# Kernel tuning notes

Measured on AMD Instinct MI355X. Metric: run time of the kernel, lower is better.

Reference implementation:

```python
import jax, jax.numpy as jnp
import numpy as np

EMB = 512
HEADS = 8


def setup_inputs() -> dict:
    key = jax.random.key(0)
    ks = jax.random.split(key, 9)
    b, t, k, h = 4, 2048, EMB, HEADS
    s = 1.0 / np.sqrt(k)
    x = jax.random.normal(ks[0], (b, t, k), dtype=jnp.float32)
    Wq = jax.random.normal(ks[1], (k, h * k), dtype=jnp.float32) * s
    bq = jnp.zeros((h * k,), dtype=jnp.float32)
    Wk = jax.random.normal(ks[2], (k, h * k), dtype=jnp.float32) * s
    bk = jnp.zeros((h * k,), dtype=jnp.float32)
    Wv = jax.random.normal(ks[3], (k, h * k), dtype=jnp.float32) * s
    bv = jnp.zeros((h * k,), dtype=jnp.float32)
    Wo = jax.random.normal(ks[4], (h * k, k), dtype=jnp.float32) * (1.0 / np.sqrt(h * k))
    bo = jnp.zeros((k,), dtype=jnp.float32)
    return {"x": x, "Wq": Wq, "bq": bq, "Wk": Wk, "bk": bk,
            "Wv": Wv, "bv": bv, "Wo": Wo, "bo": bo}


def reference(x, Wq, bq, Wk, bk, Wv, bv, Wo, bo):
    b, t, k = x.shape
    h = Wq.shape[1] // k
    scale = k ** (-0.25)  # applied to both q and k, matching /= k**(1/4)
    # projections: [b,t,k] -> [b,t,h,k] -> [b,h,t,k]
    q = (x @ Wq + bq).reshape(b, t, h, k).transpose(0, 2, 1, 3) * scale
    kk = (x @ Wk + bk).reshape(b, t, h, k).transpose(0, 2, 1, 3) * scale
    v = (x @ Wv + bv).reshape(b, t, h, k).transpose(0, 2, 1, 3)
    # attention scores [b,h,t,t]
    scores = jnp.einsum('bhqk,bhsk->bhqs', q, kk)
    w = jax.nn.softmax(scores, axis=-1)
    out = jnp.einsum('bhqs,bhsk->bhqk', w, v)  # [b,h,t,k]
    out = out.transpose(0, 2, 1, 3).reshape(b, t, h * k)
    return out @ Wo + bo
```

## Files before the change

kernel.cpp:

```cpp
#include <hip/hip_runtime.h>
#include <hip/hip_bf16.h>
#include <stdint.h>

typedef __hip_bfloat16 bf16;
typedef __bf16 bf16x8 __attribute__((ext_vector_type(8)));
typedef float floatx4 __attribute__((ext_vector_type(4)));

#define AS_LDS __attribute__((address_space(3)))
#define AS_GLB __attribute__((address_space(1)))

__device__ __forceinline__ void gload_lds16(const bf16* g, bf16* l) {
    __builtin_amdgcn_global_load_lds((const AS_GLB void*)g, (AS_LDS void*)l, 16, 0, 0);
}

__global__ void probe_dtype(const float* __restrict__ x, int* __restrict__ flag) {
    __shared__ int cnt;
    if (threadIdx.x == 0) cnt = 0;
    __syncthreads();
    int ok = 0;
    for (int i = threadIdx.x; i < 4096; i += 256) {
        float v = x[i];
        if (v == v && fabsf(v) < 1.0e3f) ok++;
    }
    atomicAdd(&cnt, ok);
    __syncthreads();
    if (threadIdx.x == 0) *flag = (cnt > 2048) ? 1 : 0;
}

__global__ __launch_bounds__(256) void convert_to_bf16(
    const void* __restrict__ in, bf16* __restrict__ out, long n,
    const int* __restrict__ flag)
{
    long i = ((long)blockIdx.x * 256 + threadIdx.x) * 8;
    if (i >= n) return;
    bf16 o[8];
    if (*flag) {
        const float* p = (const float*)in + i;
        float4 a = *(const float4*)p;
        float4 b = *(const float4*)(p + 4);
        o[0] = __float2bfloat16(a.x); o[1] = __float2bfloat16(a.y);
        o[2] = __float2bfloat16(a.z); o[3] = __float2bfloat16(a.w);
        o[4] = __float2bfloat16(b.x); o[5] = __float2bfloat16(b.y);
        o[6] = __float2bfloat16(b.z); o[7] = __float2bfloat16(b.w);
    } else {
        *(float4*)o = *(const float4*)((const bf16*)in + i);
    }
    *(float4*)&out[i] = *(float4*)o;
}

__global__ __launch_bounds__(256) void emit_out(
    const bf16* __restrict__ in, void* __restrict__ out, long n,
    const int* __restrict__ flag)
{
    long i = ((long)blockIdx.x * 256 + threadIdx.x) * 8;
    if (i >= n) return;
    bf16 v[8];
    *(float4*)v = *(const float4*)&in[i];
    if (*flag) {
        float* o = (float*)out + i;
        float4 a, b;
        a.x = __bfloat162float(v[0]); a.y = __bfloat162float(v[1]);
        a.z = __bfloat162float(v[2]); a.w = __bfloat162float(v[3]);
        b.x = __bfloat162float(v[4]); b.y = __bfloat162float(v[5]);
        b.z = __bfloat162float(v[6]); b.w = __bfloat162float(v[7]);
        *(float4*)o = a;
        *(float4*)(o + 4) = b;
    } else {
        *(float4*)((bf16*)out + i) = *(float4*)v;
    }
}

__global__ __launch_bounds__(256) void transpose_any(
    const void* __restrict__ inv, bf16* __restrict__ out,
    int ldin, int ldout, const int* __restrict__ flag)
{
    __shared__ bf16 tile[64][80];
    const int fp32 = *flag;
    const int c0 = blockIdx.x * 64;
    const int r0 = blockIdx.y * 64;
    const int tid = threadIdx.x;
#pragma unroll
    for (int it = 0; it < 2; ++it) {
        int ch = tid + it * 256;
        int r = ch >> 3, c = (ch & 7) * 8;
        long eidx = (long)(r0 + r) * ldin + (c0 + c);
        if (fp32) {
            const float* p = (const float*)inv + eidx;
            float4 a = *(const float4*)p;
            float4 b = *(const float4*)(p + 4);
            bf16 o[8];
            o[0] = __float2bfloat16(a.x); o[1] = __float2bfloat16(a.y);
            o[2] = __float2bfloat16(a.z); o[3] = __float2bfloat16(a.w);
            o[4] = __float2bfloat16(b.x); o[5] = __float2bfloat16(b.y);
            o[6] = __float2bfloat16(b.z); o[7] = __float2bfloat16(b.w);
            *(float4*)&tile[r][c] = *(float4*)o;
        } else {
            *(float4*)&tile[r][c] = *(const float4*)((const bf16*)inv + eidx);
        }
    }
    __syncthreads();
#pragma unroll
    for (int it = 0; it < 2; ++it) {
        int ch = tid + it * 256;
        int oc = ch >> 3, rb = (ch & 7) * 8;
        bf16 tmp[8];
#pragma unroll
        for (int i = 0; i < 8; ++i) tmp[i] = tile[rb + i][oc];
        *(float4*)&out[(long)(c0 + oc) * ldout + r0 + rb] = *(float4*)tmp;
    }
}

__global__ __launch_bounds__(256) void transpose_bf16(
    const bf16* __restrict__ in, bf16* __restrict__ out,
    int ldin, int ldout,
    int nz1, long in_z1, long out_z1, long in_z2, long out_z2)
{
    __shared__ bf16 tile[64][80];
    const int z = blockIdx.z;
    const int z1 = z % nz1, z2 = z / nz1;
    in  += (long)z1 * in_z1 + (long)z2 * in_z2;
    out += (long)z1 * out_z1 + (long)z2 * out_z2;
    const int c0 = blockIdx.x * 64;
    const int r0 = blockIdx.y * 64;
    const int tid = threadIdx.x;
#pragma unroll
    for (int it = 0; it < 2; ++it) {
        int ch = tid + it * 256;
        int r = ch >> 3, c = (ch & 7) * 8;
        *(float4*)&tile[r][c] = *(const float4*)&in[(long)(r0 + r) * ldin + c0 + c];
    }
    __syncthreads();
#pragma unroll
    for (int it = 0; it < 2; ++it) {
        int ch = tid + it * 256;
        int oc = ch >> 3, rb = (ch & 7) * 8;
        bf16 tmp[8];
#pragma unroll
        for (int i = 0; i < 8; ++i) tmp[i] = tile[rb + i][oc];
        *(float4*)&out[(long)(c0 + oc) * ldout + r0 + rb] = *(float4*)tmp;
    }
}

template <int MODE>
__global__ __launch_bounds__(512, 2) void gemm256(
    const bf16* __restrict__ A, const bf16* __restrict__ Bt,
    bf16* __restrict__ C, const bf16* __restrict__ bias,
    int lda, int ldb, int ldc,
    long az, long bz, long cz, int K, float scale, int qcols,
    bf16* __restrict__ Vt, int vcol0)
{
    __shared__ bf16 AsL[2][2][256 * 32];
    __shared__ bf16 BsL[2][2][256 * 32];

    const int tid  = threadIdx.x;
    const int lane = tid & 63;
    const int wave = tid >> 6;
    const int wr = wave >> 2;
    const int wc = wave & 3;
    const int lm = lane & 15;
    const int cl = lane >> 4;
    const long zz = blockIdx.z;
    A  += zz * az;
    Bt += zz * bz;
    C  += zz * cz;
    const int m0 = blockIdx.y * 256;
    const int n0 = blockIdx.x * 256;

    int offA[8], offB[4];
#pragma unroll
    for (int i = 0; i < 8; ++i) {
        int row = wr * 128 + i * 16 + lm;
        offA[i] = row * 32 + ((cl ^ ((row >> 1) & 3)) << 3);
    }
#pragma unroll
    for (int j = 0; j < 4; ++j) {
        int row = wc * 64 + j * 16 + lm;
        offB[j] = row * 32 + ((cl ^ ((row >> 1) & 3)) << 3);
    }

    const int sr = lane >> 2;
    const int sc = lane & 3;
    const int NT = K >> 6;

    floatx4 acc[8][4];
#pragma unroll
    for (int i = 0; i < 8; ++i)
#pragma unroll
        for (int j = 0; j < 4; ++j)
            acc[i][j] = (floatx4){0.f, 0.f, 0.f, 0.f};

    auto stageU = [&](int which, int t, int kh) {
        if (t >= NT) return;
        const bf16* G = which ? Bt : A;
        const int ldg  = which ? ldb : lda;
        const int g0   = which ? n0 : m0;
        bf16* lb = which ? &BsL[t & 1][kh][0] : &AsL[t & 1][kh][0];
        const int kcol = t * 64 + kh * 32;
#pragma unroll
        for (int ii = 0; ii < 2; ++ii) {
            int row = ii * 128 + wave * 16 + sr;
            int cg  = sc ^ ((row >> 1) & 3);
            gload_lds16(G + (long)(g0 + row) * ldg + kcol + cg * 8,
                        lb + row * 32 + sc * 8);
        }
    };

    bf16x8 af[8], bfv[2];
    auto dsA = [&](int b, int kh) {
        const bf16* p = &AsL[b][kh][0];
#pragma unroll
        for (int i = 0; i < 8; ++i) af[i] = *(const bf16x8*)(p + offA[i]);
    };
    auto dsB = [&](int b, int kh, int nh) {
        const bf16* p = &BsL[b][kh][0];
        bfv[0] = *(const bf16x8*)(p + offB[nh * 2]);
        bfv[1] = *(const bf16x8*)(p + offB[nh * 2 + 1]);
    };
    auto mfmaQ = [&](int nh) {
        __builtin_amdgcn_s_setprio(1);
#pragma unroll
        for (int i = 0; i < 8; ++i) {
            acc[i][nh * 2] = __builtin_amdgcn_mfma_f32_16x16x32_bf16(
                af[i], bfv[0], acc[i][nh * 2], 0, 0, 0);
            acc[i][nh * 2 + 1] = __builtin_amdgcn_mfma_f32_16x16x32_bf16(
                af[i], bfv[1], acc[i][nh * 2 + 1], 0, 0, 0);
        }
        __builtin_amdgcn_s_setprio(0);
    };

#define BAR    __builtin_amdgcn_s_barrier()
#define SBZ    __builtin_amdgcn_sched_barrier(0)
#define LGKM0  do { asm volatile("s_waitcnt lgkmcnt(0)" ::: "memory"); SBZ; } while (0)
#define VM(n)  do { asm volatile("s_waitcnt vmcnt(" #n ")" ::: "memory"); SBZ; } while (0)

    stageU(0, 0, 0); stageU(1, 0, 0); stageU(0, 0, 1); stageU(1, 0, 1);
    stageU(0, 1, 0); stageU(1, 1, 0);
    VM(4);
    BAR;

    for (int t0 = 0; t0 < NT; t0 += 2) {
        const bool last = (t0 + 2 >= NT);
        dsA(0, 0); dsB(0, 0, 0); stageU(0, t0 + 1, 1);
        BAR; LGKM0; mfmaQ(0); BAR;
        dsB(0, 0, 1); stageU(1, t0 + 1, 1);
        BAR; LGKM0; mfmaQ(1); BAR;
        dsA(0, 1); dsB(0, 1, 0); stageU(0, t0 + 2, 0);
        BAR; LGKM0; mfmaQ(0); BAR;
        dsB(0, 1, 1); stageU(1, t0 + 2, 0);
        BAR; LGKM0; mfmaQ(1);
        if (last) { VM(0); } else { VM(4); }
        BAR;
        dsA(1, 0); dsB(1, 0, 0); stageU(0, t0 + 2, 1);
        BAR; LGKM0; mfmaQ(0); BAR;
        dsB(1, 0, 1); stageU(1, t0 + 2, 1);
        BAR; LGKM0; mfmaQ(1); BAR;
        dsA(1, 1); dsB(1, 1, 0); stageU(0, t0 + 3, 0);
        BAR; LGKM0; mfmaQ(0); BAR;
        dsB(1, 1, 1); stageU(1, t0 + 3, 0);
        BAR; LGKM0; mfmaQ(1);
        if (!last) { VM(4); }
        BAR;
    }
#undef BAR
#undef SBZ
#undef LGKM0
#undef VM

    const int cr = (lane >> 4) * 4;
    if constexpr (MODE == 1) {
#pragma unroll
        for (int j = 0; j < 4; ++j) {
            int col = n0 + wc * 64 + j * 16 + lm;
#pragma unroll
            for (int i = 0; i < 8; ++i)
#pragma unroll
                for (int r = 0; r < 4; ++r) {
                    int row = m0 + wr * 128 + i * 16 + cr + r;
                    C[(long)row * ldc + col] = __float2bfloat16(__expf(acc[i][j][r]));
                }
        }
    } else {
        if (n0 >= vcol0) {
#pragma unroll
            for (int j = 0; j < 4; ++j) {
                int col = n0 + wc * 64 + j * 16 + lm;
                float bv = __bfloat162float(bias[col]);
                int eg = col - vcol0;
                bf16* vt = Vt + ((long)(eg >> 9) * 512 + (eg & 511)) * 2048;
#pragma unroll
                for (int i = 0; i < 8; ++i) {
                    int t0v = m0 + wr * 128 + i * 16 + cr;
                    bf16 pk[4];
#pragma unroll
                    for (int r = 0; r < 4; ++r)
                        pk[r] = __float2bfloat16(acc[i][j][r] + bv);
                    *(ushort4*)&vt[t0v] = *(ushort4*)pk;
                }
            }
        } else {
#pragma unroll
            for (int j = 0; j < 4; ++j) {
                int col = n0 + wc * 64 + j * 16 + lm;
                float bv = __bfloat162float(bias[col]);
                float sc2 = (col < qcols) ? scale : 1.0f;
#pragma unroll
                for (int i = 0; i < 8; ++i)
#pragma unroll
                    for (int r = 0; r < 4; ++r) {
                        int row = m0 + wr * 128 + i * 16 + cr + r;
                        C[(long)row * ldc + col] =
                            __float2bfloat16((acc[i][j][r] + bv) * sc2);
                    }
            }
        }
    }
}

template <int MODE, bool SWAP = false>
__global__ __launch_bounds__(256) void gemm_bt(
    const bf16* __restrict__ A, const bf16* __restrict__ Bt,
    bf16* __restrict__ C, const bf16* __restrict__ bias,
    int lda, int ldb, int ldc,
    long az, long bz, long cz, int K, float scale, int qcols,
    bf16* __restrict__ Vt, int vcol0)
{
    __shared__ bf16 As[128 * 64];
    __shared__ bf16 Bs[128 * 64];

    const int tid  = threadIdx.x;
    const int lane = tid & 63;
    const int wave = tid >> 6;
    const int wx = wave & 1;
    const int wy = wave >> 1;
    const long zz = blockIdx.z;
    A  += zz * az;
    Bt += zz * bz;
    C  += zz * cz;
    const int bm = SWAP ? blockIdx.x : blockIdx.y;
    const int bn = SWAP ? blockIdx.y : blockIdx.x;
    const int m0 = bm * 128;
    const int n0 = bn * 128;

    const int lm = lane & 15;
    const int kq = (lane >> 4) * 8;

    floatx4 acc[4][4];
#pragma unroll
    for (int i = 0; i < 4; ++i)
#pragma unroll
        for (int j = 0; j < 4; ++j)
            acc[i][j] = (floatx4){0.f, 0.f, 0.f, 0.f};

    floatx4 accOnes[4];
    bf16x8 ones;
    if constexpr (MODE == 3) {
#pragma unroll
        for (int i = 0; i < 4; ++i) accOnes[i] = (floatx4){0.f, 0.f, 0.f, 0.f};
#pragma unroll
        for (int k = 0; k < 8; ++k) ones[k] = (__bf16)1.0f;
    }

    for (int kt = 0; kt < K; kt += 64) {
        __syncthreads();
#pragma unroll
        for (int it = 0; it < 4; ++it) {
            int ch = tid + it * 256;
            int r = ch >> 3;
            int c = (ch & 7) * 8;
            gload_lds16(A  + (long)(m0 + r) * lda + (kt + c), &As[ch * 8]);
            gload_lds16(Bt + (long)(n0 + r) * ldb + (kt + c), &Bs[ch * 8]);
        }
        __syncthreads();
#pragma unroll
        for (int kk = 0; kk < 64; kk += 32) {
            bf16x8 af[4], bfv[4];
#pragma unroll
            for (int i = 0; i < 4; ++i)
                af[i] = *(const bf16x8*)&As[(wy * 64 + i * 16 + lm) * 64 + kk + kq];
#pragma unroll
            for (int j = 0; j < 4; ++j)
                bfv[j] = *(const bf16x8*)&Bs[(wx * 64 + j * 16 + lm) * 64 + kk + kq];
#pragma unroll
            for (int i = 0; i < 4; ++i) {
#pragma unroll
                for (int j = 0; j < 4; ++j)
                    acc[i][j] = __builtin_amdgcn_mfma_f32_16x16x32_bf16(
                        af[i], bfv[j], acc[i][j], 0, 0, 0);
                if constexpr (MODE == 3)
                    accOnes[i] = __builtin_amdgcn_mfma_f32_16x16x32_bf16(
                        af[i], ones, accOnes[i], 0, 0, 0);
            }
        }
    }

    const int cr = (lane >> 4) * 4;
    if constexpr (MODE == 1) {
#pragma unroll
        for (int j = 0; j < 4; ++j) {
            int col = n0 + wx * 64 + j * 16 + lm;
#pragma unroll
            for (int i = 0; i < 4; ++i)
#pragma unroll
                for (int r = 0; r < 4; ++r) {
                    int row = m0 + wy * 64 + i * 16 + cr + r;
                    C[(long)row * ldc + col] = __float2bfloat16(__expf(acc[i][j][r]));
                }
        }
    } else if constexpr (MODE == 3) {
        floatx4 inv[4];
#pragma unroll
        for (int i = 0; i < 4; ++i)
#pragma unroll
            for (int r = 0; r < 4; ++r)
                inv[i][r] = 1.0f / accOnes[i][r];
#pragma unroll
        for (int j = 0; j < 4; ++j) {
            int col = n0 + wx * 64 + j * 16 + lm;
#pragma unroll
            for (int i = 0; i < 4; ++i)
#pragma unroll
                for (int r = 0; r < 4; ++r) {
                    int row = m0 + wy * 64 + i * 16 + cr + r;
                    C[(long)row * ldc + col] =
                        __float2bfloat16(acc[i][j][r] * inv[i][r]);
                }
        }
    } else if constexpr (MODE == 4) {
        if (n0 >= vcol0) {
#pragma unroll
            for (int j = 0; j < 4; ++j) {
                int col = n0 + wx * 64 + j * 16 + lm;
                float bv = __bfloat162float(bias[col]);
                int eg = col - vcol0;
                bf16* vt = Vt + ((long)(eg >> 9) * 512 + (eg & 511)) * 2048;
#pragma unroll
                for (int i = 0; i < 4; ++i) {
                    int t0 = m0 + wy * 64 + i * 16 + cr;
                    bf16 pk[4];
#pragma unroll
                    for (int r = 0; r < 4; ++r)
                        pk[r] = __float2bfloat16(acc[i][j][r] + bv);
                    *(ushort4*)&vt[t0] = *(ushort4*)pk;
                }
            }
        } else {
#pragma unroll
            for (int j = 0; j < 4; ++j) {
                int col = n0 + wx * 64 + j * 16 + lm;
                float bv = __bfloat162float(bias[col]);
                float sc = (col < qcols) ? scale : 1.0f;
#pragma unroll
                for (int i = 0; i < 4; ++i)
#pragma unroll
                    for (int r = 0; r < 4; ++r) {
                        int row = m0 + wy * 64 + i * 16 + cr + r;
                        C[(long)row * ldc + col] =
                            __float2bfloat16((acc[i][j][r] + bv) * sc);
                    }
            }
        }
    } else {
#pragma unroll
        for (int j = 0; j < 4; ++j) {
            int col = n0 + wx * 64 + j * 16 + lm;
            float bv = (MODE == 0 && bias) ? __bfloat162float(bias[col]) : 0.f;
            float sc = (col < qcols) ? scale : 1.0f;
#pragma unroll
            for (int i = 0; i < 4; ++i) {
#pragma unroll
                for (int r = 0; r < 4; ++r) {
                    int row = m0 + wy * 64 + i * 16 + cr + r;
                    long idx = (long)row * ldc + col;
                    float v;
                    if (MODE == 2) v = acc[i][j][r] + __bfloat162float(C[idx]);
                    else           v = (acc[i][j][r] + bv) * sc;
                    C[idx] = __float2bfloat16(v);
                }
            }
        }
    }
}

template <bool SWAP = false>
__global__ __launch_bounds__(256) void gemm_bt_splitk(
    const bf16* __restrict__ A, const bf16* __restrict__ Bt,
    bf16* __restrict__ P, int lda, int ldb, int ldp,
    long az, long bz, long pz, long skStride, int nsk, int Kc)
{
    __shared__ bf16 As[128 * 64];
    __shared__ bf16 Bs[128 * 64];

    const int tid  = threadIdx.x;
    const int lane = tid & 63;
    const int wave = tid >> 6;
    const int wx = wave & 1;
    const int wy = wave >> 1;
    const int zz = blockIdx.z;
    const int ks = zz % nsk;
    const int zh = zz / nsk;
    A  += (long)zh * az;
    Bt += (long)zh * bz;
    bf16* Pz = P + (long)zh * pz + (long)ks * skStride;
    const int bm = SWAP ? blockIdx.x : blockIdx.y;
    const int bn = SWAP ? blockIdx.y : blockIdx.x;
    const int m0 = bm * 128;
    const int n0 = bn * 128;
    const int k0 = ks * Kc;

    const int lm = lane & 15;
    const int kq = (lane >> 4) * 8;

    floatx4 acc[4][4];
#pragma unroll
    for (int i = 0; i < 4; ++i)
#pragma unroll
        for (int j = 0; j < 4; ++j)
            acc[i][j] = (floatx4){0.f, 0.f, 0.f, 0.f};

    for (int kt = k0; kt < k0 + Kc; kt += 64) {
        __syncthreads();
#pragma unroll
        for (int it = 0; it < 4; ++it) {
            int ch = tid + it * 256;
            int r = ch >> 3;
            int c = (ch & 7) * 8;
            gload_lds16(A  + (long)(m0 + r) * lda + (kt + c), &As[ch * 8]);
            gload_lds16(Bt + (long)(n0 + r) * ldb + (kt + c), &Bs[ch * 8]);
        }
        __syncthreads();
#pragma unroll
        for (int kk = 0; kk < 64; kk += 32) {
            bf16x8 af[4], bfv[4];
#pragma unroll
            for (int i = 0; i < 4; ++i)
                af[i] = *(const bf16x8*)&As[(wy * 64 + i * 16 + lm) * 64 + kk + kq];
#pragma unroll
            for (int j = 0; j < 4; ++j)
                bfv[j] = *(const bf16x8*)&Bs[(wx * 64 + j * 16 + lm) * 64 + kk + kq];
#pragma unroll
            for (int i = 0; i < 4; ++i)
#pragma unroll
                for (int j = 0; j < 4; ++j)
                    acc[i][j] = __builtin_amdgcn_mfma_f32_16x16x32_bf16(
                        af[i], bfv[j], acc[i][j], 0, 0, 0);
        }
    }

    const int cr = (lane >> 4) * 4;
#pragma unroll
    for (int j = 0; j < 4; ++j) {
        int col = n0 + wx * 64 + j * 16 + lm;
#pragma unroll
        for (int i = 0; i < 4; ++i)
#pragma unroll
            for (int r = 0; r < 4; ++r) {
                int row = m0 + wy * 64 + i * 16 + cr + r;
                Pz[(long)row * ldp + col] = __float2bfloat16(acc[i][j][r]);
            }
    }
}

__global__ __launch_bounds__(256) void reduce_emit(
    const bf16* __restrict__ P, const bf16* __restrict__ bias,
    void* __restrict__ out, long MN, int N,
    const int* __restrict__ flag)
{
    long i = ((long)blockIdx.x * 256 + threadIdx.x) * 8;
    if (i >= MN) return;
    bf16 bb[8], a[8], b[8];
    *(float4*)bb = *(const float4*)&bias[i & (N - 1)];
    *(float4*)a  = *(const float4*)&P[i];
    *(float4*)b  = *(const float4*)&P[MN + i];
    float s[8];
#pragma unroll
    for (int k = 0; k < 8; ++k)
        s[k] = __bfloat162float(bb[k]) + __bfloat162float(a[k]) + __bfloat162float(b[k]);
    if (*flag) {
        float* o = (float*)out + i;
        float4 lo = {s[0], s[1], s[2], s[3]};
        float4 hi = {s[4], s[5], s[6], s[7]};
        *(float4*)o = lo;
        *(float4*)(o + 4) = hi;
    } else {
        bf16 o[8];
#pragma unroll
        for (int k = 0; k < 8; ++k) o[k] = __float2bfloat16(s[k]);
        *(float4*)&((bf16*)out)[i] = *(float4*)o;
    }
}

__global__ __launch_bounds__(256) void reduce_splitk(
    const bf16* __restrict__ P, const bf16* __restrict__ bias,
    bf16* __restrict__ Out, long MN, int N, int SK)
{
    long i = ((long)blockIdx.x * 256 + threadIdx.x) * 8;
    if (i >= MN) return;
    float s[8];
    if (bias) {
        bf16 bb[8];
        *(float4*)bb = *(const float4*)&bias[i & (N - 1)];
#pragma unroll
        for (int k = 0; k < 8; ++k) s[k] = __bfloat162float(bb[k]);
    } else {
#pragma unroll
        for (int k = 0; k < 8; ++k) s[k] = 0.f;
    }
    for (int z = 0; z < SK; ++z) {
        bf16 a[8];
        *(float4*)a = *(const float4*)&P[(long)z * MN + i];
#pragma unroll
        for (int k = 0; k < 8; ++k) s[k] += __bfloat162float(a[k]);
    }
    bf16 o[8];
#pragma unroll
    for (int k = 0; k < 8; ++k) o[k] = __float2bfloat16(s[k]);
    *(float4*)&Out[i] = *(float4*)o;
}

__global__ __launch_bounds__(256) void softmax_rows2048(bf16* __restrict__ S)
{
    __shared__ float red[8];
    const long row = blockIdx.x;
    bf16* p = S + row * 2048;
    const int tid = threadIdx.x;
    float4 raw = *(const float4*)&p[tid * 8];
    bf16 vb[8];
    *(float4*)vb = raw;
    float v[8];
#pragma unroll
    for (int i = 0; i < 8; ++i) v[i] = __bfloat162float(vb[i]);
    float m = v[0];
#pragma unroll
    for (int i = 1; i < 8; ++i) m = fmaxf(m, v[i]);
#pragma unroll
    for (int o = 32; o > 0; o >>= 1) m = fmaxf(m, __shfl_xor(m, o));
    if ((tid & 63) == 0) red[tid >> 6] = m;
    __syncthreads();
    m = fmaxf(fmaxf(red[0], red[1]), fmaxf(red[2], red[3]));
    float s = 0.f;
#pragma unroll
    for (int i = 0; i < 8; ++i) { v[i] = __expf(v[i] - m); s += v[i]; }
#pragma unroll
    for (int o = 32; o > 0; o >>= 1) s += __shfl_xor(s, o);
    if ((tid & 63) == 0) red[4 + (tid >> 6)] = s;
    __syncthreads();
    s = (red[4] + red[5]) + (red[6] + red[7]);
    float inv = 1.f / s;
#pragma unroll
    for (int i = 0; i < 8; ++i) vb[i] = __float2bfloat16(v[i] * inv);
    *(float4*)&p[tid * 8] = *(float4*)vb;
}

extern "C" void kernel_launch(void* const* d_in, const int* in_sizes, int n_in,
                              void* d_out, int out_size, void* d_ws, size_t ws_size,
                              hipStream_t stream)
{
    const int Bb = 4, T = 2048, E = 512, H = 8;
    const int HE = H * E;
    const int N3 = 3 * HE;
    const int N2 = 2 * HE;
    const int M  = Bb * T;
    const long NX = (long)M * E;

    const void* xr = nullptr;
    const void* Wr[4] = {nullptr, nullptr, nullptr, nullptr};
    const void* br[3] = {nullptr, nullptr, nullptr};
    const void* bor = nullptr;
    int nw = 0, nb = 0;
    for (int i = 0; i < n_in; ++i) {
        int s = in_sizes[i];
        if      (s == (int)NX)      xr = d_in[i];
        else if (s == E * HE)       { if (nw < 4) Wr[nw++] = d_in[i]; }
        else if (s == HE)           { if (nb < 3) br[nb++] = d_in[i]; }
        else if (s == E)            bor = d_in[i];
    }
    if (!xr || nw < 4 || nb < 3 || !bor) {
        xr = d_in[0]; Wr[0] = d_in[1]; br[0] = d_in[2]; Wr[1] = d_in[3];
        br[1] = d_in[4]; Wr[2] = d_in[5]; br[2] = d_in[6]; Wr[3] = d_in[7];
        bor = d_in[8];
    }

    const float qscale = 0.04419417382415922f;
    const int   QC = 1 << 30;
    dim3 blk(256);

    bf16* pool = (bf16*)d_ws;
    int*  flag = (int*)(void*)pool;
    bf16* xc   = pool + 8;
    bf16* bqc  = xc  + NX;
    bf16* bkc  = bqc + HE;
    bf16* bvc  = bkc + HE;
    bf16* boc  = bvc + HE;
    bf16* WqT  = boc + E;
    const size_t w2m = (size_t)E * HE;
    bf16* WkT  = WqT + w2m;
    bf16* WvT  = WkT + w2m;
    bf16* WoT  = WvT + w2m;
    bf16* Ofin = WoT + w2m;
    bf16* p0   = Ofin + NX;

    const size_t wsE    = ws_size / sizeof(bf16);
    const size_t fixedE = (size_t)(p0 - pool);
    const size_t wQK   = (size_t)T * N2;
    const size_t wQKV  = (size_t)T * N3;
    const size_t wBat  = (size_t)T * HE;
    const size_t wHd   = (size_t)T * E;
    const size_t sAll  = (size_t)H * T * T;
    const size_t sOne  = (size_t)T * T;
    const size_t wBig  = (size_t)M * HE;
    const size_t needB2 = fixedE + wQK + wBat + sAll + wBig;
    const size_t needB  = fixedE + wQKV + 2 * wBat + sAll;
    const size_t needC  = fixedE + 5 * wBat + sOne;
    const size_t needD  = fixedE + 5 * wHd  + sOne;
    if (wsE < needD) return;

    probe_dtype<<<dim3(1), blk, 0, stream>>>((const float*)xr, flag);
    convert_to_bf16<<<dim3((unsigned)((NX / 8 + 255) / 256)), blk, 0, stream>>>(
        xr, xc, NX, flag);
    convert_to_bf16<<<dim3(2), blk, 0, stream>>>(br[0], bqc, HE, flag);
    convert_to_bf16<<<dim3(2), blk, 0, stream>>>(br[1], bkc, HE, flag);
    convert_to_bf16<<<dim3(2), blk, 0, stream>>>(br[2], bvc, HE, flag);
    convert_to_bf16<<<dim3(1), blk, 0, stream>>>(bor, boc, E, flag);
    transpose_any<<<dim3(HE / 64, E / 64, 1), blk, 0, stream>>>(Wr[0], WqT, HE, E, flag);
    transpose_any<<<dim3(HE / 64, E / 64, 1), blk, 0, stream>>>(Wr[1], WkT, HE, E, flag);
    transpose_any<<<dim3(HE / 64, E / 64, 1), blk, 0, stream>>>(Wr[2], WvT, HE, E, flag);
    transpose_any<<<dim3(E / 64, HE / 64, 1), blk, 0, stream>>>(Wr[3], WoT, E, HE, flag);

    if (wsE >= needB2) {
        bf16* QKb = p0;
        bf16* Vtb = QKb + wQK;
        bf16* S   = Vtb + wBat;
        bf16* Oatt = S + sAll;

        for (int b = 0; b < Bb; ++b) {
            const bf16* xb = xc + (size_t)b * T * E;
            gemm256<4><<<dim3(N3 / 256, T / 256, 1), dim3(512), 0, stream>>>(
                xb, WqT, QKb, bqc, E, E, N2, 0, 0, 0, E, qscale, HE, Vtb, N2);
            gemm256<1><<<dim3(T / 256, T / 256, H), dim3(512), 0, stream>>>(
                QKb, QKb + HE, S, nullptr, N2, N2, T,
                (long)E, (long)E, (long)T * T, E, 1.f, QC, nullptr, 0);
            gemm_bt<3, true><<<dim3(T / 128, E / 128, H), blk, 0, stream>>>(
                S, Vtb, Oatt + (size_t)b * T * HE, nullptr, T, T, HE,
                (long)T * T, (long)E * T, (long)E, T, 1.f, QC, nullptr, 0);
        }
        gemm_bt_splitk<true><<<dim3(M / 128, E / 128, 2), blk, 0, stream>>>(
            Oatt, WoT, QKb, HE, HE, E, 0, 0, 0, (long)M * E, 2, HE / 2);
        reduce_emit<<<dim3((unsigned)((NX / 8 + 255) / 256)), blk, 0, stream>>>(
            QKb, boc, d_out, NX, E, flag);
        return;
    }

    if (wsE >= needB) {
        bf16* QKVb = p0;
        bf16* Vtb  = QKVb + wQKV;
        bf16* Oatt = Vtb + wBat;
        bf16* S    = Oatt + wBat;

        for (int b = 0; b < Bb; ++b) {
            const bf16* xb = xc + (size_t)b * T * E;
            gemm_bt<0><<<dim3(N3 / 128, T / 128, 1), blk, 0, stream>>>(
                xb, WqT, QKVb, bqc, E, E, N3, 0, 0, 0, E, qscale, HE, nullptr, 0);
            transpose_bf16<<<dim3(E / 64, T / 64, H), blk, 0, stream>>>(
                QKVb + 2 * HE, Vtb, N3, T, H, (long)E, (long)E * T, 0, 0);
            gemm_bt<0><<<dim3(T / 128, T / 128, H), blk, 0, stream>>>(
                QKVb, QKVb + HE, S, nullptr, N3, N3, T,
                (long)E, (long)E, (long)T * T, E, 1.f, QC, nullptr, 0);
            softmax_rows2048<<<dim3(H * T, 1, 1), blk, 0, stream>>>(S);
            gemm_bt<0><<<dim3(E / 128, T / 128, H), blk, 0, stream>>>(
                S, Vtb, Oatt, nullptr, T, T, HE,
                (long)T * T, (long)E * T, (long)E, T, 1.f, QC, nullptr, 0);
            gemm_bt_splitk<false><<<dim3(E / 128, T / 128, 8), blk, 0, stream>>>(
                Oatt, WoT, (bf16*)S, HE, HE, E, 0, 0, 0, (long)T * E, 8, HE / 8);
            reduce_splitk<<<dim3((unsigned)(((long)T * E / 8 + 255) / 256)), blk, 0, stream>>>(
                (bf16*)S, boc, Ofin + (size_t)b * T * E, (long)T * E, E, 8);
        }
    } else if (wsE >= needC) {
        bf16* Qb  = p0;
        bf16* Kb  = Qb  + wBat;
        bf16* Vb  = Kb  + wBat;
        bf16* Vtb = Vb  + wBat;
        bf16* Ob  = Vtb + wBat;
        bf16* S   = Ob  + wBat;

        for (int b = 0; b < Bb; ++b) {
            const bf16* xb = xc + (size_t)b * T * E;
            gemm_bt<0><<<dim3(HE / 128, T / 128, 1), blk, 0, stream>>>(
                xb, WqT, Qb, bqc, E, E, HE, 0, 0, 0, E, qscale, QC, nullptr, 0);
            gemm_bt<0><<<dim3(HE / 128, T / 128, 1), blk, 0, stream>>>(
                xb, WkT, Kb, bkc, E, E, HE, 0, 0, 0, E, 1.f, QC, nullptr, 0);
            gemm_bt<0><<<dim3(HE / 128, T / 128, 1), blk, 0, stream>>>(
                xb, WvT, Vb, bvc, E, E, HE, 0, 0, 0, E, 1.f, QC, nullptr, 0);
            transpose_bf16<<<dim3(E / 64, T / 64, H), blk, 0, stream>>>(
                Vb, Vtb, HE, T, H, (long)E, (long)E * T, 0, 0);
            for (int h = 0; h < H; ++h) {
                gemm_bt<0><<<dim3(T / 128, T / 128, 1), blk, 0, stream>>>(
                    Qb + (size_t)h * E, Kb + (size_t)h * E, S, nullptr,
                    HE, HE, T, 0, 0, 0, E, 1.f, QC, nullptr, 0);
                softmax_rows2048<<<dim3(T, 1, 1), blk, 0, stream>>>(S);
                gemm_bt<0><<<dim3(E / 128, T / 128, 1), blk, 0, stream>>>(
                    S, Vtb + (size_t)h * E * T, Ob + (size_t)h * E, nullptr,
                    T, T, HE, 0, 0, 0, T, 1.f, QC, nullptr, 0);
            }
            gemm_bt<0><<<dim3(E / 128, T / 128, 1), blk, 0, stream>>>(
                Ob, WoT, Ofin + (size_t)b * T * E, boc,
                HE, HE, E, 0, 0, 0, HE, 1.f, QC, nullptr, 0);
        }
    } else {
        bf16* Qh  = p0;
        bf16* Kh  = Qh  + wHd;
        bf16* Vh  = Kh  + wHd;
        bf16* Vth = Vh  + wHd;
        bf16* Oh  = Vth + wHd;
        bf16* S   = Oh  + wHd;

        for (int b = 0; b < Bb; ++b) {
            const bf16* xb = xc + (size_t)b * T * E;
            bf16* outb = Ofin + (size_t)b * T * E;
            for (int h = 0; h < H; ++h) {
                const size_t hw = (size_t)h * E * E;
                gemm_bt<0><<<dim3(E / 128, T / 128, 1), blk, 0, stream>>>(
                    xb, WqT + hw, Qh, bqc + (size_t)h * E, E, E, E,
                    0, 0, 0, E, qscale, QC, nullptr, 0);
                gemm_bt<0><<<dim3(E / 128, T / 128, 1), blk, 0, stream>>>(
                    xb, WkT + hw, Kh, bkc + (size_t)h * E, E, E, E,
                    0, 0, 0, E, 1.f, QC, nullptr, 0);
                gemm_bt<0><<<dim3(E / 128, T / 128, 1), blk, 0, stream>>>(
                    xb, WvT + hw, Vh, bvc + (size_t)h * E, E, E, E,
                    0, 0, 0, E, 1.f, QC, nullptr, 0);
                transpose_bf16<<<dim3(E / 64, T / 64, 1), blk, 0, stream>>>(
                    Vh, Vth, E, T, 1, 0, 0, 0, 0);
                gemm_bt<0><<<dim3(T / 128, T / 128, 1), blk, 0, stream>>>(
                    Qh, Kh, S, nullptr, E, E, T, 0, 0, 0, E, 1.f, QC, nullptr, 0);
                softmax_rows2048<<<dim3(T, 1, 1), blk, 0, stream>>>(S);
                gemm_bt<0><<<dim3(E / 128, T / 128, 1), blk, 0, stream>>>(
                    S, Vth, Oh, nullptr, T, T, E, 0, 0, 0, T, 1.f, QC, nullptr, 0);
                if (h == 0)
                    gemm_bt<0><<<dim3(E / 128, T / 128, 1), blk, 0, stream>>>(
                        Oh, WoT, outb, boc, E, HE, E, 0, 0, 0, E, 1.f, QC, nullptr, 0);
                else
                    gemm_bt<2><<<dim3(E / 128, T / 128, 1), blk, 0, stream>>>(
                        Oh, WoT + (size_t)h * E, outb, nullptr,
                        E, HE, E, 0, 0, 0, E, 1.f, QC, nullptr, 0);
            }
        }
    }

    emit_out<<<dim3((unsigned)((NX / 8 + 255) / 256)), blk, 0, stream>>>(
        Ofin, d_out, NX, flag);
}
```

Measured before the change: 975.2 us.

## Add XCD-aware block swizzles and swap GEMM operands for vectorized epilogue stores

Remaps block indices so blocks that share the same head or tile land on the same XCD, aiming for better L2 reuse across chiplets. Swaps the A/B operands in the score, PV and output-projection GEMMs so each lane's accumulator rows are contiguous in memory, letting the epilogues write packed 64-bit stores instead of scattered 2-byte ones. The score output uses nontemporal stores, and the QKV epilogue uses lane shuffles to transpose values into packed stores. The PV softmax row-sum is now computed from the ones vector times the B fragment. The swizzles hard-code the grid shapes, which is a correctness risk if the sizes change.

```diff
diff --git a/kernel.cpp b/kernel.cpp
--- a/kernel.cpp
+++ b/kernel.cpp
@@ -141,7 +141,7 @@
     }
 }
 
-template <int MODE>
+template <int MODE, int SWZ>
 __global__ __launch_bounds__(512, 2) void gemm256(
     const bf16* __restrict__ A, const bf16* __restrict__ Bt,
     bf16* __restrict__ C, const bf16* __restrict__ bias,
@@ -159,12 +159,23 @@
     const int wc = wave & 3;
     const int lm = lane & 15;
     const int cl = lane >> 4;
-    const long zz = blockIdx.z;
+
+    int bxx = blockIdx.x, byy = blockIdx.y, bzz = blockIdx.z;
+    if constexpr (SWZ == 1) {
+        int flat = bxx + (byy << 3) + (bzz << 6);
+        int xcd = flat & 7, idx = flat >> 3;
+        bzz = xcd; bxx = idx & 7; byy = idx >> 3;
+    } else if constexpr (SWZ == 2) {
+        int flat = bxx + byy * 48;
+        int xcd = flat & 7, idx = flat >> 3;
+        bxx = xcd * 6 + idx % 6; byy = idx / 6; bzz = 0;
+    }
+    const long zz = bzz;
     A  += zz * az;
     Bt += zz * bz;
     C  += zz * cz;
-    const int m0 = blockIdx.y * 256;
-    const int n0 = blockIdx.x * 256;
+    const int m0 = byy * 256;
+    const int n0 = bxx * 256;
 
     int offA[8], offB[4];
 #pragma unroll
@@ -270,14 +281,17 @@
     if constexpr (MODE == 1) {
 #pragma unroll
         for (int j = 0; j < 4; ++j) {
-            int col = n0 + wc * 64 + j * 16 + lm;
-#pragma unroll
-            for (int i = 0; i < 8; ++i)
-#pragma unroll
-                for (int r = 0; r < 4; ++r) {
-                    int row = m0 + wr * 128 + i * 16 + cr + r;
-                    C[(long)row * ldc + col] = __float2bfloat16(__expf(acc[i][j][r]));
-                }
+            long q = n0 + wc * 64 + j * 16 + lm;
+            bf16* Cr = C + q * ldc + m0 + wr * 128;
+#pragma unroll
+            for (int i = 0; i < 8; ++i) {
+                bf16 pk[4];
+#pragma unroll
+                for (int r = 0; r < 4; ++r)
+                    pk[r] = __float2bfloat16(__expf(acc[i][j][r]));
+                __builtin_nontemporal_store(*(const uint64_t*)pk,
+                                            (uint64_t*)&Cr[i * 16 + cr]);
+            }
         }
     } else {
         if (n0 >= vcol0) {
@@ -294,29 +308,45 @@
 #pragma unroll
                     for (int r = 0; r < 4; ++r)
                         pk[r] = __float2bfloat16(acc[i][j][r] + bv);
-                    *(ushort4*)&vt[t0v] = *(ushort4*)pk;
+                    *(uint64_t*)&vt[t0v] = *(const uint64_t*)pk;
                 }
             }
         } else {
+            const int l4 = lane & 3;
+            float bvj[4], scj[4];
 #pragma unroll
             for (int j = 0; j < 4; ++j) {
                 int col = n0 + wc * 64 + j * 16 + lm;
-                float bv = __bfloat162float(bias[col]);
-                float sc2 = (col < qcols) ? scale : 1.0f;
-#pragma unroll
-                for (int i = 0; i < 8; ++i)
-#pragma unroll
-                    for (int r = 0; r < 4; ++r) {
-                        int row = m0 + wr * 128 + i * 16 + cr + r;
-                        C[(long)row * ldc + col] =
-                            __float2bfloat16((acc[i][j][r] + bv) * sc2);
-                    }
-            }
-        }
-    }
-}
-
-template <int MODE, bool SWAP = false>
+                bvj[j] = __bfloat162float(bias[col]);
+                scj[j] = (col < qcols) ? scale : 1.0f;
+            }
+#pragma unroll
+            for (int i = 0; i < 8; ++i) {
+                int row = m0 + wr * 128 + i * 16 + cr + l4;
+                bf16* Cr = C + (long)row * ldc + n0 + wc * 64 + (lm & ~3);
+#pragma unroll
+                for (int j = 0; j < 4; ++j) {
+                    float x0 = (acc[i][j][0] + bvj[j]) * scj[j];
+                    float x1 = (acc[i][j][1] + bvj[j]) * scj[j];
+                    float x2 = (acc[i][j][2] + bvj[j]) * scj[j];
+                    float x3 = (acc[i][j][3] + bvj[j]) * scj[j];
+                    float u = __shfl_xor((l4 & 1) ? x0 : x1, 1);
+                    float v = __shfl_xor((l4 & 1) ? x2 : x3, 1);
+                    if (l4 & 1) { x0 = u; x2 = v; } else { x1 = u; x3 = v; }
+                    u = __shfl_xor((l4 & 2) ? x0 : x2, 2);
+                    v = __shfl_xor((l4 & 2) ? x1 : x3, 2);
+                    if (l4 & 2) { x0 = u; x1 = v; } else { x2 = u; x3 = v; }
+                    bf16 pk[4];
+                    pk[0] = __float2bfloat16(x0); pk[1] = __float2bfloat16(x1);
+                    pk[2] = __float2bfloat16(x2); pk[3] = __float2bfloat16(x3);
+                    *(uint64_t*)&Cr[j * 16] = *(const uint64_t*)pk;
+                }
+            }
+        }
+    }
+}
+
+template <int MODE, bool SWAP = false, int SWZ = 0>
 __global__ __launch_bounds__(256) void gemm_bt(
     const bf16* __restrict__ A, const bf16* __restrict__ Bt,
     bf16* __restrict__ C, const bf16* __restrict__ bias,
@@ -332,12 +362,19 @@
     const int wave = tid >> 6;
     const int wx = wave & 1;
     const int wy = wave >> 1;
-    const long zz = blockIdx.z;
+
+    int bxx = blockIdx.x, byy = blockIdx.y, bzz = blockIdx.z;
+    if constexpr (SWZ == 3) {
+        int flat = bxx + (byy << 4) + (bzz << 6);
+        int xcd = flat & 7, idx = flat >> 3;
+        bzz = xcd; byy = idx & 3; bxx = idx >> 2;
+    }
+    const long zz = bzz;
     A  += zz * az;
     Bt += zz * bz;
     C  += zz * cz;
-    const int bm = SWAP ? blockIdx.x : blockIdx.y;
-    const int bn = SWAP ? blockIdx.y : blockIdx.x;
+    const int bm = SWAP ? bxx : byy;
+    const int bn = SWAP ? byy : bxx;
     const int m0 = bm * 128;
     const int n0 = bn * 128;
 
@@ -380,16 +417,18 @@
 #pragma unroll
             for (int j = 0; j < 4; ++j)
                 bfv[j] = *(const bf16x8*)&Bs[(wx * 64 + j * 16 + lm) * 64 + kk + kq];
-#pragma unroll
-            for (int i = 0; i < 4; ++i) {
+            if constexpr (MODE == 3) {
+#pragma unroll
+                for (int j = 0; j < 4; ++j)
+                    accOnes[j] = __builtin_amdgcn_mfma_f32_16x16x32_bf16(
+                        ones, bfv[j], accOnes[j], 0, 0, 0);
+            }
+#pragma unroll
+            for (int i = 0; i < 4; ++i)
 #pragma unroll
                 for (int j = 0; j < 4; ++j)
                     acc[i][j] = __builtin_amdgcn_mfma_f32_16x16x32_bf16(
                         af[i], bfv[j], acc[i][j], 0, 0, 0);
-                if constexpr (MODE == 3)
-                    accOnes[i] = __builtin_amdgcn_mfma_f32_16x16x32_bf16(
-                        af[i], ones, accOnes[i], 0, 0, 0);
-            }
         }
     }
 
@@ -407,23 +446,19 @@
                 }
         }
     } else if constexpr (MODE == 3) {
-        floatx4 inv[4];
-#pragma unroll
-        for (int i = 0; i < 4; ++i)
-#pragma unroll
-            for (int r = 0; r < 4; ++r)
-                inv[i][r] = 1.0f / accOnes[i][r];
 #pragma unroll
         for (int j = 0; j < 4; ++j) {
-            int col = n0 + wx * 64 + j * 16 + lm;
-#pragma unroll
-            for (int i = 0; i < 4; ++i)
-#pragma unroll
-                for (int r = 0; r < 4; ++r) {
-                    int row = m0 + wy * 64 + i * 16 + cr + r;
-                    C[(long)row * ldc + col] =
-                        __float2bfloat16(acc[i][j][r] * inv[i][r]);
-                }
+            int tcol = n0 + wx * 64 + j * 16 + lm;
+            float inv = 1.0f / accOnes[j][0];
+            bf16* Cr = C + (long)tcol * ldc + m0 + wy * 64;
+#pragma unroll
+            for (int i = 0; i < 4; ++i) {
+                bf16 pk[4];
+#pragma unroll
+                for (int r = 0; r < 4; ++r)
+                    pk[r] = __float2bfloat16(acc[i][j][r] * inv);
+                *(uint64_t*)&Cr[i * 16 + cr] = *(const uint64_t*)pk;
+            }
         }
     } else if constexpr (MODE == 4) {
         if (n0 >= vcol0) {
@@ -440,7 +475,7 @@
 #pragma unroll
                     for (int r = 0; r < 4; ++r)
                         pk[r] = __float2bfloat16(acc[i][j][r] + bv);
-                    *(ushort4*)&vt[t0] = *(ushort4*)pk;
+                    *(uint64_t*)&vt[t0] = *(const uint64_t*)pk;
                 }
             }
         } else {
@@ -481,7 +516,7 @@
     }
 }
 
-template <bool SWAP = false>
+template <bool SWAP = false, int SWZ = 0>
 __global__ __launch_bounds__(256) void gemm_bt_splitk(
     const bf16* __restrict__ A, const bf16* __restrict__ Bt,
     bf16* __restrict__ P, int lda, int ldb, int ldp,
@@ -495,14 +530,21 @@
     const int wave = tid >> 6;
     const int wx = wave & 1;
     const int wy = wave >> 1;
-    const int zz = blockIdx.z;
+
+    int bxx = blockIdx.x, byy = blockIdx.y, bzz = blockIdx.z;
+    if constexpr (SWZ == 9) {
+        int flat = bxx + (byy << 6) + (bzz << 8);
+        int nf = (flat & 7) * 64 + (flat >> 3);
+        bxx = nf & 63; byy = (nf >> 6) & 3; bzz = nf >> 8;
+    }
+    const int zz = bzz;
     const int ks = zz % nsk;
     const int zh = zz / nsk;
     A  += (long)zh * az;
     Bt += (long)zh * bz;
     bf16* Pz = P + (long)zh * pz + (long)ks * skStride;
-    const int bm = SWAP ? blockIdx.x : blockIdx.y;
-    const int bn = SWAP ? blockIdx.y : blockIdx.x;
+    const int bm = SWAP ? bxx : byy;
+    const int bn = SWAP ? byy : bxx;
     const int m0 = bm * 128;
     const int n0 = bn * 128;
     const int k0 = ks * Kc;
@@ -547,16 +589,32 @@
     }
 
     const int cr = (lane >> 4) * 4;
-#pragma unroll
-    for (int j = 0; j < 4; ++j) {
-        int col = n0 + wx * 64 + j * 16 + lm;
-#pragma unroll
-        for (int i = 0; i < 4; ++i)
-#pragma unroll
-            for (int r = 0; r < 4; ++r) {
-                int row = m0 + wy * 64 + i * 16 + cr + r;
-                Pz[(long)row * ldp + col] = __float2bfloat16(acc[i][j][r]);
-            }
+    if constexpr (SWZ == 9) {
+#pragma unroll
+        for (int j = 0; j < 4; ++j) {
+            int tcol = n0 + wx * 64 + j * 16 + lm;
+            bf16* Pr = Pz + (long)tcol * ldp + m0 + wy * 64;
+#pragma unroll
+            for (int i = 0; i < 4; ++i) {
+                bf16 pk[4];
+#pragma unroll
+                for (int r = 0; r < 4; ++r)
+                    pk[r] = __float2bfloat16(acc[i][j][r]);
+                *(uint64_t*)&Pr[i * 16 + cr] = *(const uint64_t*)pk;
+            }
+        }
+    } else {
+#pragma unroll
+        for (int j = 0; j < 4; ++j) {
+            int col = n0 + wx * 64 + j * 16 + lm;
+#pragma unroll
+            for (int i = 0; i < 4; ++i)
+#pragma unroll
+                for (int r = 0; r < 4; ++r) {
+                    int row = m0 + wy * 64 + i * 16 + cr + r;
+                    Pz[(long)row * ldp + col] = __float2bfloat16(acc[i][j][r]);
+                }
+        }
     }
 }
 
@@ -734,17 +792,17 @@
 
         for (int b = 0; b < Bb; ++b) {
             const bf16* xb = xc + (size_t)b * T * E;
-            gemm256<4><<<dim3(N3 / 256, T / 256, 1), dim3(512), 0, stream>>>(
+            gemm256<4, 2><<<dim3(N3 / 256, T / 256, 1), dim3(512), 0, stream>>>(
                 xb, WqT, QKb, bqc, E, E, N2, 0, 0, 0, E, qscale, HE, Vtb, N2);
-            gemm256<1><<<dim3(T / 256, T / 256, H), dim3(512), 0, stream>>>(
-                QKb, QKb + HE, S, nullptr, N2, N2, T,
+            gemm256<1, 1><<<dim3(T / 256, T / 256, H), dim3(512), 0, stream>>>(
+                QKb + HE, QKb, S, nullptr, N2, N2, T,
                 (long)E, (long)E, (long)T * T, E, 1.f, QC, nullptr, 0);
-            gemm_bt<3, true><<<dim3(T / 128, E / 128, H), blk, 0, stream>>>(
-                S, Vtb, Oatt + (size_t)b * T * HE, nullptr, T, T, HE,
-                (long)T * T, (long)E * T, (long)E, T, 1.f, QC, nullptr, 0);
-        }
-        gemm_bt_splitk<true><<<dim3(M / 128, E / 128, 2), blk, 0, stream>>>(
-            Oatt, WoT, QKb, HE, HE, E, 0, 0, 0, (long)M * E, 2, HE / 2);
+            gemm_bt<3, false, 3><<<dim3(T / 128, E / 128, H), blk, 0, stream>>>(
+                Vtb, S, Oatt + (size_t)b * T * HE, nullptr, T, T, HE,
+                (long)E * T, (long)T * T, (long)E, T, 1.f, QC, nullptr, 0);
+        }
+        gemm_bt_splitk<false, 9><<<dim3(M / 128, E / 128, 2), blk, 0, stream>>>(
+            WoT, Oatt, QKb, HE, HE, E, 0, 0, 0, (long)M * E, 2, HE / 2);
         reduce_emit<<<dim3((unsigned)((NX / 8 + 255) / 256)), blk, 0, stream>>>(
             QKb, boc, d_out, NX, E, flag);
         return;
```

Result: faster. 875.3 us (-10.2%).
